# Kernel tuning notes

Hardware: AMD Instinct MI355X
Metric: run time of the kernel (lower is better)

## Reference

```python
import jax, jax.numpy as jnp
import numpy as np

CAPACITY_FACTOR = 1.2


def setup_inputs() -> dict:
    key = jax.random.key(0)
    k1, k2 = jax.random.split(key, 2)
    D, E = 1024, 64
    x = jax.random.normal(k1, (8, 4096, D), dtype=jnp.float32)
    # xavier-uniform-ish router weight, zero bias (as in __init__)
    limit = np.sqrt(6.0 / (D + E)).astype(np.float32)
    W = jax.random.uniform(k2, (E, D), dtype=jnp.float32, minval=-limit, maxval=limit)
    b = jnp.zeros((E,), dtype=jnp.float32)
    return {"x": x, "W": W, "b": b, "detach_inputs": 0}


def reference(x, W, b, detach_inputs):
    bsz, seqlen, D = x.shape
    E = W.shape[0]                      # num experts == max_steps
    N = bsz * seqlen                    # num tokens
    x_flat = x.reshape(N, D)
    if detach_inputs:
        x_flat = jax.lax.stop_gradient(x_flat)
    logits = x_flat @ W.T + b           # [N, E]

    # expert-choice capacity (static python ints)
    k = max(1, int(N / max(1, E) * CAPACITY_FACTOR))
    k = min(k, N)

    # per-expert top-k over tokens: [E, k]
    topk_vals, topk_idx = jax.lax.top_k(logits.T, k)
    cand_tok = topk_idx.reshape(-1)                       # [E*k] token ids
    cand_exp = jnp.repeat(jnp.arange(E, dtype=jnp.int32), k)  # [E*k]
    cand_val = topk_vals.reshape(-1)                      # [E*k]

    # scatter-amax: best candidate logit per token (torch scatter_reduce_ 'amax')
    best_val = jnp.full((N,), -jnp.inf, dtype=logits.dtype).at[cand_tok].max(cand_val)

    # candidates that achieve the per-token max; dedup -> one expert per token
    # (tie-break: smallest expert index, matching first-occurrence after sort)
    eq = cand_val == best_val[cand_tok]
    exp_cand = jnp.where(eq, cand_exp, E).astype(jnp.int32)
    token_exp = jnp.full((N,), E, dtype=jnp.int32).at[cand_tok].min(exp_cand)
    selected = token_exp < E                              # token was picked by some expert
    assigned_expert = jnp.where(selected, token_exp, -1)  # [N], -1 = unassigned

    # load-balance loss from per-expert counts (bincount of assigned experts)
    sel_f = selected.astype(logits.dtype)
    counts = jnp.zeros((E,), dtype=logits.dtype).at[jnp.where(selected, token_exp, 0)].add(sel_f)
    mean_load = counts.mean()
    load_balance_loss = ((counts - mean_load) ** 2).mean() / (mean_load + 1e-9)

    best_val_out = jnp.where(selected, best_val, jnp.zeros((), logits.dtype))
    return (best_val_out, assigned_expert, selected, load_balance_loss)
```

## Files before the change

### kernel.cpp

```cpp
#include <hip/hip_runtime.h>
#include <math.h>

typedef __attribute__((ext_vector_type(4))) double d4;

__device__ inline unsigned fkey(float f) {
  unsigned bits = __float_as_uint(f);
  return (bits & 0x80000000u) ? ~bits : (bits | 0x80000000u);
}

#define STORE4D(base, off, v)                          \
  {                                                    \
    double* _p = (base) + (off);                       \
    _p[0] = (double)(v).x; _p[1] = (double)(v).y;      \
    _p[2] = (double)(v).z; _p[3] = (double)(v).w;      \
  }

__global__ __launch_bounds__(512, 4) void logits_fused_kernel(
    const float* __restrict__ x, const float* __restrict__ W,
    const float* __restrict__ bias, float* __restrict__ logits,
    float* __restrict__ logitsT, int N, int D) {
  __shared__ __attribute__((aligned(16))) double xbuf[2][64 * 33];
  __shared__ __attribute__((aligned(16))) double wbuf[2][64 * 33];
  __shared__ unsigned s_fl;

  const int tid = threadIdx.x;
  const int tok0 = blockIdx.x * 64;
  const int l = tid & 63;
  const int l15 = l & 15;
  const int lk = l >> 4;

  double* pA = &wbuf[0][0];
  double* pB = &wbuf[0][64];
  if (tid < 64) {
    pA[l15 * 4 + lk] = (double)(l15 * 4 + lk + 1);
    pB[lk * 16 + l15] = (double)(l15 * 7 + lk * 3 + 2);
  }
  __syncthreads();
  if (tid < 64) {
    double a = pA[l15 * 4 + lk];
    double b = pB[lk * 16 + l15];
    d4 pacc = (d4)0.0;
    pacc = __builtin_amdgcn_mfma_f64_16x16x4f64(a, b, pacc, 0, 0, 0);
    unsigned res = 4;
    for (int m = 3; m >= 0; --m) {
      bool ok = true;
#pragma unroll
      for (int i = 0; i < 4; ++i) {
        int tr_ = (m < 2) ? ((m == 0) ? 4 * lk + i : lk + 4 * i) : l15;
        int tc_ = (m < 2) ? l15 : ((m == 2) ? 4 * lk + i : lk + 4 * i);
        double ref = 0.0;
#pragma unroll
        for (int kk = 0; kk < 4; ++kk) ref += pA[tr_ * 4 + kk] * pB[kk * 16 + tc_];
        ok = ok && (pacc[i] == ref);
      }
      if (__all(ok)) res = (unsigned)m;
    }
    if (l == 0) s_fl = res;
  }
  __syncthreads();
  const unsigned fl = s_fl;
  __syncthreads();

  if (fl < 4u) {
    const int w = tid >> 6;
    const int rb = (w & 3) * 16;
    const int cb = (w >> 2) * 32;

    d4 acc0 = (d4)0.0;
    d4 acc1 = (d4)0.0;

    const int srow = tid >> 3;
    const int sc = tid & 7;
    const float* gx = x + (size_t)(tok0 + srow) * D + sc * 4;
    const float* gw = W + (size_t)srow * D + sc * 4;
    const int lo = srow * 33 + sc * 4;

    const int nch = D >> 5;
    const int xa0 = (rb + l15) * 33 + lk;
    const int ba0 = (cb + l15) * 33 + lk;

    float4 rx = *(const float4*)gx;
    float4 rw = *(const float4*)gw;
    STORE4D(&xbuf[0][0], lo, rx);
    STORE4D(&wbuf[0][0], lo, rw);
    if (nch > 1) {
      rx = *(const float4*)(gx + 32);
      rw = *(const float4*)(gw + 32);
    }
    __syncthreads();

    for (int c = 0; c < nch; ++c) {
      const int cbuf = c & 1;
      const int nb = cbuf ^ 1;
      if (c + 1 < nch) {
        STORE4D(&xbuf[nb][0], lo, rx);
        STORE4D(&wbuf[nb][0], lo, rw);
        if (c + 2 < nch) {
          rx = *(const float4*)(gx + (c + 2) * 32);
          rw = *(const float4*)(gw + (c + 2) * 32);
        }
      }
      const double* xr = &xbuf[cbuf][0];
      const double* wr = &wbuf[cbuf][0];
      double a[8], b0[8], b1[8];
#pragma unroll
      for (int s = 0; s < 8; ++s) {
        a[s]  = xr[xa0 + 4 * s];
        b0[s] = wr[ba0 + 4 * s];
        b1[s] = wr[ba0 + 16 * 33 + 4 * s];
      }
#pragma unroll
      for (int s = 0; s < 8; ++s) {
        acc0 = __builtin_amdgcn_mfma_f64_16x16x4f64(a[s], b0[s], acc0, 0, 0, 0);
        acc1 = __builtin_amdgcn_mfma_f64_16x16x4f64(a[s], b1[s], acc1, 0, 0, 0);
      }
      __syncthreads();
    }

    float* ls = (float*)&xbuf[0][0];
#pragma unroll
    for (int ct = 0; ct < 2; ++ct) {
      const d4* ac = (ct == 0) ? &acc0 : &acc1;
#pragma unroll
      for (int i = 0; i < 4; ++i) {
        int tr_, tc_;
        if (fl < 2u) { tc_ = l15; tr_ = (fl == 0u) ? 4 * lk + i : lk + 4 * i; }
        else         { tr_ = l15; tc_ = (fl == 2u) ? 4 * lk + i : lk + 4 * i; }
        int col = cb + ct * 16 + tc_;
        ls[(rb + tr_) * 68 + col] = (float)((*ac)[i] + (double)bias[col]);
      }
    }
    __syncthreads();
#pragma unroll
    for (int it = 0; it < 2; ++it) {
      int slot = it * 512 + tid;
      int row = slot >> 4, c4 = slot & 15;
      float4 v = {ls[row * 68 + c4 * 4 + 0], ls[row * 68 + c4 * 4 + 1],
                  ls[row * 68 + c4 * 4 + 2], ls[row * 68 + c4 * 4 + 3]};
      *(float4*)(logits + (size_t)(tok0 + row) * 64 + c4 * 4) = v;
    }
#pragma unroll
    for (int it = 0; it < 2; ++it) {
      int slot = it * 512 + tid;
      int e = slot >> 4, t4 = slot & 15;
      float4 v = {ls[(t4 * 4 + 0) * 68 + e], ls[(t4 * 4 + 1) * 68 + e],
                  ls[(t4 * 4 + 2) * 68 + e], ls[(t4 * 4 + 3) * 68 + e]};
      *(float4*)(logitsT + (size_t)e * N + tok0 + t4 * 4) = v;
    }
  } else {
    for (int o = tid; o < 64 * 64; o += 512) {
      int row = o >> 6, col = o & 63;
      const float* xp = x + (size_t)(tok0 + row) * D;
      const float* wp = W + (size_t)col * D;
      double s = 0.0;
      for (int kk = 0; kk < D; ++kk)
        s = fma((double)xp[kk], (double)wp[kk], s);
      float v = (float)(s + (double)bias[col]);
      logits[(size_t)(tok0 + row) * 64 + col] = v;
      logitsT[(size_t)col * N + tok0 + row] = v;
    }
  }
}

template <int KPT4>
__global__ __launch_bounds__(1024) void select_kernel(
    const float* __restrict__ logitsT, unsigned* __restrict__ ukeys,
    int N, int k) {
  __shared__ unsigned hist[16][256];
  __shared__ unsigned s_prefix, s_rem;
  const int e = blockIdx.x;
  const int tid = threadIdx.x;
  const int wid = tid >> 6;

  const float4* src = (const float4*)(logitsT + (size_t)e * N);
  unsigned key[KPT4 > 0 ? KPT4 * 4 : 4];
  if (KPT4 > 0) {
#pragma unroll
    for (int i = 0; i < (KPT4 > 0 ? KPT4 : 1); ++i) {
      float4 v = src[tid + i * 1024];
      key[i * 4 + 0] = fkey(v.x);
      key[i * 4 + 1] = fkey(v.y);
      key[i * 4 + 2] = fkey(v.z);
      key[i * 4 + 3] = fkey(v.w);
    }
  }
  if (tid == 0) { s_prefix = 0u; s_rem = (unsigned)k; }

  for (int r = 0; r < 4; ++r) {
    const int shift = 24 - 8 * r;
    const unsigned maskhi = (r == 0) ? 0u : (0xFFFFFFFFu << (shift + 8));
#pragma unroll
    for (int z = 0; z < 4; ++z) ((unsigned*)hist)[z * 1024 + tid] = 0u;
    __syncthreads();
    const unsigned prefix = s_prefix;
    if (KPT4 > 0) {
#pragma unroll
      for (int i = 0; i < (KPT4 > 0 ? KPT4 * 4 : 1); ++i) {
        unsigned u = key[i];
        if ((u & maskhi) == prefix)
          atomicAdd(&hist[wid][(u >> shift) & 255u], 1u);
      }
    } else {
      for (int i = tid; i < (N >> 2); i += 1024) {
        float4 v = src[i];
        unsigned u0 = fkey(v.x), u1 = fkey(v.y), u2 = fkey(v.z), u3 = fkey(v.w);
        if ((u0 & maskhi) == prefix) atomicAdd(&hist[wid][(u0 >> shift) & 255u], 1u);
        if ((u1 & maskhi) == prefix) atomicAdd(&hist[wid][(u1 >> shift) & 255u], 1u);
        if ((u2 & maskhi) == prefix) atomicAdd(&hist[wid][(u2 >> shift) & 255u], 1u);
        if ((u3 & maskhi) == prefix) atomicAdd(&hist[wid][(u3 >> shift) & 255u], 1u);
      }
    }
    __syncthreads();
    if (tid < 64) {
      unsigned rem = s_rem;
      unsigned h0 = 0, h1 = 0, h2 = 0, h3 = 0;
#pragma unroll
      for (int w = 0; w < 16; ++w) {
        h0 += hist[w][tid * 4 + 0];
        h1 += hist[w][tid * 4 + 1];
        h2 += hist[w][tid * 4 + 2];
        h3 += hist[w][tid * 4 + 3];
      }
      unsigned c3 = h3, c2 = c3 + h2, c1 = c2 + h1, c0 = c1 + h0;
      unsigned cum = c0;
#pragma unroll
      for (int off = 1; off < 64; off <<= 1) {
        unsigned v = __shfl_down(cum, off);
        if (tid + off < 64) cum += v;
      }
      unsigned above = cum - c0;
      if (above < rem && rem <= cum) {
        int j; unsigned abv;
        if (above + c3 >= rem)      { j = 3; abv = above; }
        else if (above + c2 >= rem) { j = 2; abv = above + c3; }
        else if (above + c1 >= rem) { j = 1; abv = above + c2; }
        else                        { j = 0; abv = above + c1; }
        s_rem = rem - abv;
        s_prefix = prefix | ((unsigned)(tid * 4 + j) << shift);
      }
    }
    __syncthreads();
  }
  if (tid == 0) ukeys[e] = s_prefix;
}

__global__ __launch_bounds__(256) void assign_kernel(
    const float* __restrict__ logits, const unsigned* __restrict__ ukeys,
    float* __restrict__ out, int N) {
  const int lane = threadIdx.x & 63;
  const int token = blockIdx.x * 4 + (threadIdx.x >> 6);

  float v = logits[(size_t)token * 64 + lane];
  unsigned u = fkey(v);
  bool cand = (u >= ukeys[lane]);
  float cv = cand ? v : -INFINITY;
  float m = cv;
#pragma unroll
  for (int off = 32; off; off >>= 1) m = fmaxf(m, __shfl_xor(m, off));
  unsigned long long mask = __ballot(cand && (v == m));
  bool sel = (mask != 0ull);
  int minexp = sel ? (__ffsll((long long)mask) - 1) : -1;

  if (lane == 0) {
    out[token] = sel ? m : 0.0f;
    out[N + token] = (float)minexp;
    out[2 * N + token] = sel ? 1.0f : 0.0f;
  }
}

__global__ __launch_bounds__(1024) void count_loss_kernel(
    const float* __restrict__ assigned, float* __restrict__ out, int N) {
  __shared__ unsigned hist[16][64];
  const int tid = threadIdx.x;
  const int wid = tid >> 6;
  hist[wid][tid & 63] = 0u;
  __syncthreads();
  const float4* src = (const float4*)assigned;
  for (int i = tid; i < (N >> 2); i += 1024) {
    float4 v = src[i];
    int e0 = (int)v.x, e1 = (int)v.y, e2 = (int)v.z, e3 = (int)v.w;
    if (e0 >= 0) atomicAdd(&hist[wid][e0], 1u);
    if (e1 >= 0) atomicAdd(&hist[wid][e1], 1u);
    if (e2 >= 0) atomicAdd(&hist[wid][e2], 1u);
    if (e3 >= 0) atomicAdd(&hist[wid][e3], 1u);
  }
  __syncthreads();
  if (tid < 64) {
    unsigned c = 0;
#pragma unroll
    for (int w = 0; w < 16; ++w) c += hist[w][tid];
    double cd = (double)c;
    double s = cd;
#pragma unroll
    for (int off = 32; off; off >>= 1) s += __shfl_xor(s, off);
    double mean = s / 64.0;
    double d = cd - mean;
    d = d * d;
#pragma unroll
    for (int off = 32; off; off >>= 1) d += __shfl_xor(d, off);
    if (tid == 0) out[3 * (size_t)N] = (float)((d / 64.0) / (mean + 1e-9));
  }
}

extern "C" void kernel_launch(void* const* d_in, const int* in_sizes, int n_in,
                              void* d_out, int out_size, void* d_ws, size_t ws_size,
                              hipStream_t stream) {
  const float* x = (const float*)d_in[0];
  const float* W = (const float*)d_in[1];
  const float* b = (const float*)d_in[2];

  const int E = in_sizes[2];
  const int D = in_sizes[1] / E;
  const int N = in_sizes[0] / D;

  int k = (int)((double)N / (double)(E > 1 ? E : 1) * 1.2);
  if (k < 1) k = 1;
  if (k > N) k = N;

  const size_t NE = (size_t)N * E;
  float* out = (float*)d_out;

  float* logits = (float*)d_ws;
  float* logitsT = logits + NE;
  unsigned* ukeys = (unsigned*)(logitsT + NE);

  logits_fused_kernel<<<N / 64, 512, 0, stream>>>(x, W, b, logits, logitsT,
                                                  N, D);
  if (N == 32768)
    select_kernel<8><<<64, 1024, 0, stream>>>(logitsT, ukeys, N, k);
  else
    select_kernel<0><<<64, 1024, 0, stream>>>(logitsT, ukeys, N, k);
  assign_kernel<<<N / 4, 256, 0, stream>>>(logits, ukeys, out, N);
  count_loss_kernel<<<1, 1024, 0, stream>>>(out + N, out, N);
}
```

Measured before the change: 111.8 us.

## Fuse select, assign and loss into one cooperative grid-synced kernel

Replaces the three tail kernels (per-expert radix top-k threshold, per-token assignment, count/loss) with a single cooperative kernel of 64 blocks that uses grid-wide syncs between phases. Per-expert counts are accumulated in shared memory and then with global atomics. The aim is to remove the launch overhead and global round trips between the tail kernels. In exchange, the assignment phase runs on only 64 blocks of 512 active threads, which may limit parallelism compared with the previous N/4-block assign kernel.

```diff
diff --git a/kernel.cpp b/kernel.cpp
--- a/kernel.cpp
+++ b/kernel.cpp
@@ -1,5 +1,8 @@
 #include <hip/hip_runtime.h>
+#include <hip/hip_cooperative_groups.h>
 #include <math.h>
+
+namespace cg = cooperative_groups;
 
 typedef __attribute__((ext_vector_type(4))) double d4;
 
@@ -162,6 +165,118 @@
   }
 }
 
+__global__ __launch_bounds__(1024) void tail_coop_kernel(
+    const float* __restrict__ logitsT, float* __restrict__ out,
+    unsigned* __restrict__ ukeys, unsigned* __restrict__ gz,
+    int N, int k) {
+  __shared__ unsigned hist[16][256];
+  __shared__ unsigned s_prefix, s_rem;
+  __shared__ unsigned uk_lds[64];
+  __shared__ unsigned cnt[64];
+  const int e = blockIdx.x;
+  const int tid = threadIdx.x;
+  const int wid = tid >> 6;
+
+  if (e == 0 && tid < 65) gz[tid] = 0u;
+
+  const float4* src = (const float4*)(logitsT + (size_t)e * N);
+  unsigned key[32];
+#pragma unroll
+  for (int i = 0; i < 8; ++i) {
+    float4 v = src[tid + i * 1024];
+    key[i * 4 + 0] = fkey(v.x);
+    key[i * 4 + 1] = fkey(v.y);
+    key[i * 4 + 2] = fkey(v.z);
+    key[i * 4 + 3] = fkey(v.w);
+  }
+  if (tid == 0) { s_prefix = 0u; s_rem = (unsigned)k; }
+
+  for (int r = 0; r < 4; ++r) {
+    const int shift = 24 - 8 * r;
+    const unsigned maskhi = (r == 0) ? 0u : (0xFFFFFFFFu << (shift + 8));
+#pragma unroll
+    for (int z = 0; z < 4; ++z) ((unsigned*)hist)[z * 1024 + tid] = 0u;
+    __syncthreads();
+    const unsigned prefix = s_prefix;
+#pragma unroll
+    for (int i = 0; i < 32; ++i) {
+      unsigned u = key[i];
+      if ((u & maskhi) == prefix)
+        atomicAdd(&hist[wid][(u >> shift) & 255u], 1u);
+    }
+    __syncthreads();
+    if (tid < 64) {
+      unsigned rem = s_rem;
+      unsigned h0 = 0, h1 = 0, h2 = 0, h3 = 0;
+#pragma unroll
+      for (int w = 0; w < 16; ++w) {
+        h0 += hist[w][tid * 4 + 0];
+        h1 += hist[w][tid * 4 + 1];
+        h2 += hist[w][tid * 4 + 2];
+        h3 += hist[w][tid * 4 + 3];
+      }
+      unsigned c3 = h3, c2 = c3 + h2, c1 = c2 + h1, c0 = c1 + h0;
+      unsigned cum = c0;
+#pragma unroll
+      for (int off = 1; off < 64; off <<= 1) {
+        unsigned v = __shfl_down(cum, off);
+        if (tid + off < 64) cum += v;
+      }
+      unsigned above = cum - c0;
+      if (above < rem && rem <= cum) {
+        int j; unsigned abv;
+        if (above + c3 >= rem)      { j = 3; abv = above; }
+        else if (above + c2 >= rem) { j = 2; abv = above + c3; }
+        else if (above + c1 >= rem) { j = 1; abv = above + c2; }
+        else                        { j = 0; abv = above + c1; }
+        s_rem = rem - abv;
+        s_prefix = prefix | ((unsigned)(tid * 4 + j) << shift);
+      }
+    }
+    __syncthreads();
+  }
+  if (tid == 0) ukeys[e] = s_prefix;
+  __threadfence();
+  cg::this_grid().sync();
+
+  if (tid < 64) { uk_lds[tid] = ukeys[tid]; cnt[tid] = 0u; }
+  __syncthreads();
+  if (tid < 512) {
+    const int token = blockIdx.x * 512 + tid;
+    unsigned bu = 0u; int be = -1; float bv = 0.0f;
+#pragma unroll 8
+    for (int ee = 0; ee < 64; ++ee) {
+      float v = logitsT[(size_t)ee * N + token];
+      unsigned u = fkey(v);
+      unsigned uu = (u >= uk_lds[ee]) ? u : 0u;
+      if (uu > bu) { bu = uu; be = ee; bv = v; }
+    }
+    const bool sel = (bu != 0u);
+    out[token] = sel ? bv : 0.0f;
+    out[N + token] = (float)be;
+    out[2 * N + token] = sel ? 1.0f : 0.0f;
+    if (sel) atomicAdd(&cnt[be], 1u);
+  }
+  __syncthreads();
+  if (tid < 64 && cnt[tid]) atomicAdd(&gz[tid], cnt[tid]);
+  __threadfence();
+  cg::this_grid().sync();
+
+  if (blockIdx.x == 0 && tid < 64) {
+    unsigned c = atomicAdd(&gz[tid], 0u);
+    double cd = (double)c;
+    double s = cd;
+#pragma unroll
+    for (int off = 32; off; off >>= 1) s += __shfl_xor(s, off);
+    double mean = s / 64.0;
+    double d = cd - mean;
+    d = d * d;
+#pragma unroll
+    for (int off = 32; off; off >>= 1) d += __shfl_xor(d, off);
+    if (tid == 0) out[3 * (size_t)N] = (float)((d / 64.0) / (mean + 1e-9));
+  }
+}
+
 template <int KPT4>
 __global__ __launch_bounds__(1024) void select_kernel(
     const float* __restrict__ logitsT, unsigned* __restrict__ ukeys,
@@ -323,13 +438,25 @@
   float* logits = (float*)d_ws;
   float* logitsT = logits + NE;
   unsigned* ukeys = (unsigned*)(logitsT + NE);
+  unsigned* gz = ukeys + 64;
 
   logits_fused_kernel<<<N / 64, 512, 0, stream>>>(x, W, b, logits, logitsT,
                                                   N, D);
-  if (N == 32768)
-    select_kernel<8><<<64, 1024, 0, stream>>>(logitsT, ukeys, N, k);
-  else
-    select_kernel<0><<<64, 1024, 0, stream>>>(logitsT, ukeys, N, k);
-  assign_kernel<<<N / 4, 256, 0, stream>>>(logits, ukeys, out, N);
-  count_loss_kernel<<<1, 1024, 0, stream>>>(out + N, out, N);
-}
+
+  bool coop_done = false;
+  if (N == 32768 && E == 64) {
+    void* args[] = {(void*)&logitsT, (void*)&out, (void*)&ukeys,
+                    (void*)&gz, (void*)&N, (void*)&k};
+    hipError_t err = hipLaunchCooperativeKernel(
+        (const void*)tail_coop_kernel, dim3(64), dim3(1024), args, 0, stream);
+    if (err == hipSuccess) coop_done = true;
+  }
+  if (!coop_done) {
+    if (N == 32768)
+      select_kernel<8><<<64, 1024, 0, stream>>>(logitsT, ukeys, N, k);
+    else
+      select_kernel<0><<<64, 1024, 0, stream>>>(logitsT, ukeys, N, k);
+    assign_kernel<<<N / 4, 256, 0, stream>>>(logits, ukeys, out, N);
+    count_loss_kernel<<<1, 1024, 0, stream>>>(out + N, out, N);
+  }
+}
```

After: 169.0 us. 1.51x slower.
